# Performance work log

Measured on AMD Instinct MI355X. Metric: run time of the kernel, lower is better.

Reference implementation:

```python
import jax, jax.numpy as jnp
import numpy as np

ROUTINGS = 3
EPS = 1e-9

def squash(s, axis=-1):
    s2 = jnp.sum(s * s, axis=axis, keepdims=True)
    scale = s2 / (1.0 + s2 + EPS)
    return scale * s / jnp.sqrt(s2 + EPS)

def setup_inputs() -> dict:
    key = jax.random.key(0)
    k1, k2 = jax.random.split(key)
    B, N_in, D_in = 64, 2048, 16
    N_out, D_out = 32, 32
    x = jax.random.normal(k1, (B, N_in, D_in), dtype=jnp.float32)
    # glorot-uniform-ish init for W [1, N_in, N_out, D_out, D_in]
    limit = np.sqrt(6.0 / (D_in + D_out)).astype(np.float32)
    W = jax.random.uniform(k2, (1, N_in, N_out, D_out, D_in), dtype=jnp.float32,
                           minval=-limit, maxval=limit)
    return {"x": x, "W": W}

def reference(x, W):
    # u_hat[b,i,j,d] = sum_k W[0,i,j,d,k] * x[b,i,k]   -> [B, N_in, N_out, D_out]
    u_hat = jnp.einsum('bik,ijdk->bijd', x, W[0])
    b = jnp.zeros(u_hat.shape[:-1], dtype=u_hat.dtype)  # [B, N_in, N_out]
    v = None
    for i in range(ROUTINGS):
        c = jax.nn.softmax(b, axis=2)                     # softmax over output capsules
        s = jnp.einsum('bij,bijd->bjd', c, u_hat)         # [B, N_out, D_out]
        v = squash(s)
        if i < ROUTINGS - 1:
            b = b + jnp.einsum('bijd,bjd->bij', u_hat, v)  # agreement update
    return v
```

## Files before the change

### kernel.cpp

```cpp
#include <hip/hip_runtime.h>
#include <cstdint>
#include <cstddef>

#define B_   64
#define NI   2048
#define DI   16
#define NO   32
#define JD   1024
#define IT   16
#define NBX  (NI/IT)
#define XSTR 260
#define EPSQ 1e-9f

typedef __attribute__((ext_vector_type(8)))  short bf16x8;
typedef __attribute__((ext_vector_type(16))) float f32x16;

__device__ __forceinline__ uint32_t pack_split(float w) {
  uint32_t u = __float_as_uint(w);
  float hf = __uint_as_float(u & 0xffff0000u);
  uint32_t lo = __float_as_uint(w - hf) >> 16;
  return (u & 0xffff0000u) | lo;
}

__device__ __forceinline__ void cvt8(const float4 a, const float4 b, bf16x8& h8, bf16x8& l8) {
  float w[8] = {a.x, a.y, a.z, a.w, b.x, b.y, b.z, b.w};
  #pragma unroll
  for (int e = 0; e < 8; ++e) {
    uint32_t u = __float_as_uint(w[e]);
    float hf = __uint_as_float(u & 0xffff0000u);
    h8[e] = (short)(u >> 16);
    l8[e] = (short)(__float_as_uint(w[e] - hf) >> 16);
  }
}

__device__ __forceinline__ f32x16 zero16() {
  f32x16 z;
  #pragma unroll
  for (int r = 0; r < 16; ++r) z[r] = 0.0f;
  return z;
}

template<bool ROUTE>
__global__ __launch_bounds__(512, 2)
void caps_pass(const float* __restrict__ x, const float* __restrict__ W,
               const float* __restrict__ vin, float* __restrict__ part)
{
  __shared__ uint32_t xl[32 * XSTR];
  __shared__ float al[NO * 32];
  __shared__ float cl[NO * 32];

  const int t    = threadIdx.x;
  const int wv   = t >> 6;
  const int l    = t & 63;
  const int col  = l & 31;
  const int hb   = l >> 5;
  const int p    = blockIdx.x;
  const int half = blockIdx.y;
  const int i0   = p * IT;
  const int b0   = half * 32;

  for (int idx = t; idx < 32 * 64; idx += 512) {
    const int bb = idx >> 6, c4 = idx & 63;
    const float4 xv = *reinterpret_cast<const float4*>(
        x + (size_t)(b0 + bb) * (NI * DI) + (size_t)i0 * DI + (c4 << 2));
    uint4 o;
    o.x = pack_split(xv.x); o.y = pack_split(xv.y);
    o.z = pack_split(xv.z); o.w = pack_split(xv.w);
    *reinterpret_cast<uint4*>(&xl[bb * XSTR + (c4 << 2)]) = o;
  }

  float vreg[4][16];
  if constexpr (ROUTE) {
    #pragma unroll
    for (int m = 0; m < 4; ++m)
      #pragma unroll
      for (int r = 0; r < 16; ++r) {
        const int row = (r & 3) + 8 * (r >> 2) + 4 * hb;
        vreg[m][r] = vin[(size_t)(b0 + col) * JD + wv * 128 + m * 32 + row];
      }
  }

  f32x16 sacc[4];
  #pragma unroll
  for (int m = 0; m < 4; ++m) sacc[m] = zero16();

  __syncthreads();

  if constexpr (!ROUTE) {
    for (int ii = 0; ii < IT; ++ii) {
      const uint4 q0 = *reinterpret_cast<const uint4*>(&xl[col * XSTR + (ii << 4) + (hb << 3)]);
      const uint4 q1 = *reinterpret_cast<const uint4*>(&xl[col * XSTR + (ii << 4) + (hb << 3) + 4]);
      bf16x8 xh, xo;
      const uint32_t qq[8] = {q0.x, q0.y, q0.z, q0.w, q1.x, q1.y, q1.z, q1.w};
      #pragma unroll
      for (int e = 0; e < 8; ++e) { xh[e] = (short)(qq[e] >> 16); xo[e] = (short)(qq[e] & 0xffff); }

      const float* wbase = W + (size_t)(i0 + ii) * (JD * DI) + (size_t)wv * 128 * DI;
      #pragma unroll
      for (int m = 0; m < 4; ++m) {
        const float* wt = wbase + m * 32 * DI + col * DI + (hb << 3);
        const float4 wa = *reinterpret_cast<const float4*>(wt);
        const float4 wb = *reinterpret_cast<const float4*>(wt + 4);
        bf16x8 wh, wl; cvt8(wa, wb, wh, wl);
        sacc[m] = __builtin_amdgcn_mfma_f32_32x32x16_bf16(wh, xh, sacc[m], 0, 0, 0);
        sacc[m] = __builtin_amdgcn_mfma_f32_32x32x16_bf16(wh, xo, sacc[m], 0, 0, 0);
        sacc[m] = __builtin_amdgcn_mfma_f32_32x32x16_bf16(wl, xh, sacc[m], 0, 0, 0);
      }
    }
  } else {
    #pragma unroll 1
    for (int ii = 0; ii < IT; ++ii) {
      const uint4 q0 = *reinterpret_cast<const uint4*>(&xl[col * XSTR + (ii << 4) + (hb << 3)]);
      const uint4 q1 = *reinterpret_cast<const uint4*>(&xl[col * XSTR + (ii << 4) + (hb << 3) + 4]);
      bf16x8 xh, xo;
      const uint32_t qq[8] = {q0.x, q0.y, q0.z, q0.w, q1.x, q1.y, q1.z, q1.w};
      #pragma unroll
      for (int e = 0; e < 8; ++e) { xh[e] = (short)(qq[e] >> 16); xo[e] = (short)(qq[e] & 0xffff); }

      const float* wbase = W + (size_t)(i0 + ii) * (JD * DI) + (size_t)wv * 128 * DI;
      f32x16 u[4];
      #pragma unroll
      for (int m = 0; m < 4; ++m) {
        const float* wt = wbase + m * 32 * DI + col * DI + (hb << 3);
        const float4 wa = *reinterpret_cast<const float4*>(wt);
        const float4 wb = *reinterpret_cast<const float4*>(wt + 4);
        bf16x8 wh, wl; cvt8(wa, wb, wh, wl);
        f32x16 c = zero16();
        c = __builtin_amdgcn_mfma_f32_32x32x16_bf16(wh, xh, c, 0, 0, 0);
        c = __builtin_amdgcn_mfma_f32_32x32x16_bf16(wh, xo, c, 0, 0, 0);
        c = __builtin_amdgcn_mfma_f32_32x32x16_bf16(wl, xh, c, 0, 0, 0);
        u[m] = c;
      }

      float ap[4];
      #pragma unroll
      for (int m = 0; m < 4; ++m) {
        float s = 0.f;
        #pragma unroll
        for (int r = 0; r < 16; ++r) s += u[m][r] * vreg[m][r];
        s += __shfl_xor(s, 32);
        ap[m] = s;
      }
      if (l < 32) {
        #pragma unroll
        for (int m = 0; m < 4; ++m) {
          const int j = (wv << 2) + m;
          al[(j << 5) + ((col + j) & 31)] = ap[m];
        }
      }
      __syncthreads();

      {
        const int jj = t & 31;
        #pragma unroll
        for (int rd = 0; rd < 2; ++rd) {
          const int bb = (t >> 5) + (rd << 4);
          const float av = al[(jj << 5) + ((bb + jj) & 31)];
          float mx = av;
          #pragma unroll
          for (int s = 1; s < 32; s <<= 1) mx = fmaxf(mx, __shfl_xor(mx, s, 32));
          const float e = __expf(av - mx);
          float den = e;
          #pragma unroll
          for (int s = 1; s < 32; s <<= 1) den += __shfl_xor(den, s, 32);
          cl[(jj << 5) + ((bb + jj) & 31)] = e / den;
        }
      }
      __syncthreads();

      #pragma unroll
      for (int m = 0; m < 4; ++m) {
        const int j = (wv << 2) + m;
        const float cv = cl[(j << 5) + ((col + j) & 31)];
        #pragma unroll
        for (int r = 0; r < 16; ++r) sacc[m][r] += cv * u[m][r];
      }
    }
  }

  #pragma unroll
  for (int m = 0; m < 4; ++m)
    #pragma unroll
    for (int g = 0; g < 4; ++g) {
      const int jd = (wv << 7) + (m << 5) + (g << 3) + (hb << 2);
      *reinterpret_cast<float4*>(part + (((size_t)(p * B_ + b0 + col)) << 10) + jd) =
          make_float4(sacc[m][4 * g], sacc[m][4 * g + 1], sacc[m][4 * g + 2], sacc[m][4 * g + 3]);
    }
}

__global__ void reduce_squash(const float* __restrict__ part,
                              const float* __restrict__ vprev,
                              float* __restrict__ out, float scale, int addPrev)
{
  const int b   = blockIdx.x;
  const int jd0 = blockIdx.y * 512 + threadIdx.x * 4;

  float4 acc[8];
  #pragma unroll
  for (int u = 0; u < 8; ++u) acc[u] = make_float4(0.f, 0.f, 0.f, 0.f);

  for (int p = 0; p < NBX; p += 8) {
    #pragma unroll
    for (int u = 0; u < 8; ++u) {
      const float4 v = *reinterpret_cast<const float4*>(
          part + (((size_t)((p + u) * B_ + b)) << 10) + jd0);
      acc[u].x += v.x; acc[u].y += v.y; acc[u].z += v.z; acc[u].w += v.w;
    }
  }
  #pragma unroll
  for (int u = 1; u < 8; ++u) {
    acc[0].x += acc[u].x; acc[0].y += acc[u].y;
    acc[0].z += acc[u].z; acc[0].w += acc[u].w;
  }

  float val[4] = {acc[0].x * scale, acc[0].y * scale, acc[0].z * scale, acc[0].w * scale};
  float sq = val[0]*val[0] + val[1]*val[1] + val[2]*val[2] + val[3]*val[3];
  #pragma unroll
  for (int w = 1; w < 8; w <<= 1) sq += __shfl_xor(sq, w, 8);

  const float f = sq / ((1.0f + sq + EPSQ) * sqrtf(sq + EPSQ));
  float4 o = make_float4(f * val[0], f * val[1], f * val[2], f * val[3]);
  if (addPrev) {
    const float4 vp = *reinterpret_cast<const float4*>(vprev + (size_t)b * JD + jd0);
    o.x += vp.x; o.y += vp.y; o.z += vp.z; o.w += vp.w;
  }
  *reinterpret_cast<float4*>(out + (size_t)b * JD + jd0) = o;
}

extern "C" void kernel_launch(void* const* d_in, const int* in_sizes, int n_in,
                              void* d_out, int out_size, void* d_ws, size_t ws_size,
                              hipStream_t stream) {
  const float* x = (const float*)d_in[0];
  const float* W = (const float*)d_in[1];
  float* ws  = (float*)d_ws;
  float* out = (float*)d_out;

  float* partb = ws;
  float* v0    = ws + (size_t)NBX * B_ * JD;
  float* vs    = v0 + B_ * JD;

  const dim3 grid(NBX, 2);
  const dim3 rgrid(B_, 2);
  caps_pass<false><<<grid, 512, 0, stream>>>(x, W, nullptr, partb);
  reduce_squash<<<rgrid, 128, 0, stream>>>(partb, nullptr, v0, 1.0f / 32.0f, 0);
  caps_pass<true><<<grid, 512, 0, stream>>>(x, W, v0, partb);
  reduce_squash<<<rgrid, 128, 0, stream>>>(partb, v0, vs, 1.0f, 1);
  caps_pass<true><<<grid, 512, 0, stream>>>(x, W, vs, partb);
  reduce_squash<<<rgrid, 128, 0, stream>>>(partb, nullptr, out, 1.0f, 0);
}
```

Baseline: 324.5 us.

## Halve input-capsule tile, reorder grid, add atomic-fold fallback for small workspace

Cuts the input capsules per block from 16 to 8, which doubles the grid to 512 blocks and is meant to fill more of the GPU's compute units. The grid is re-indexed so that neighbouring block IDs share a row slab. A fallback path for when the workspace is too small for the doubled partial buffer folds pairs of partials with atomicAdd after a memset. The trade-off is twice as many partial sums for reduce_squash to read, and possibly atomic traffic if the fallback path is taken.

```diff
diff --git a/kernel.cpp b/kernel.cpp
--- a/kernel.cpp
+++ b/kernel.cpp
@@ -7,9 +7,9 @@
 #define DI   16
 #define NO   32
 #define JD   1024
-#define IT   16
+#define IT   8
 #define NBX  (NI/IT)
-#define XSTR 260
+#define XSTR (IT*DI + 4)
 #define EPSQ 1e-9f
 
 typedef __attribute__((ext_vector_type(8)))  short bf16x8;
@@ -40,7 +40,7 @@
   return z;
 }
 
-template<bool ROUTE>
+template<bool ROUTE, bool FOLD>
 __global__ __launch_bounds__(512, 2)
 void caps_pass(const float* __restrict__ x, const float* __restrict__ W,
                const float* __restrict__ vin, float* __restrict__ part)
@@ -54,13 +54,13 @@
   const int l    = t & 63;
   const int col  = l & 31;
   const int hb   = l >> 5;
-  const int p    = blockIdx.x;
-  const int half = blockIdx.y;
+  const int half = blockIdx.x >> 3;
+  const int p    = blockIdx.y * 8 + (blockIdx.x & 7);
   const int i0   = p * IT;
   const int b0   = half * 32;
 
-  for (int idx = t; idx < 32 * 64; idx += 512) {
-    const int bb = idx >> 6, c4 = idx & 63;
+  for (int idx = t; idx < 32 * (IT * DI / 4); idx += 512) {
+    const int bb = idx / (IT * DI / 4), c4 = idx % (IT * DI / 4);
     const float4 xv = *reinterpret_cast<const float4*>(
         x + (size_t)(b0 + bb) * (NI * DI) + (size_t)i0 * DI + (c4 << 2));
     uint4 o;
@@ -178,17 +178,26 @@
     }
   }
 
+  const int pslot = FOLD ? (p >> 1) : p;
   #pragma unroll
   for (int m = 0; m < 4; ++m)
     #pragma unroll
     for (int g = 0; g < 4; ++g) {
       const int jd = (wv << 7) + (m << 5) + (g << 3) + (hb << 2);
-      *reinterpret_cast<float4*>(part + (((size_t)(p * B_ + b0 + col)) << 10) + jd) =
-          make_float4(sacc[m][4 * g], sacc[m][4 * g + 1], sacc[m][4 * g + 2], sacc[m][4 * g + 3]);
-    }
-}
-
-__global__ void reduce_squash(const float* __restrict__ part,
+      float* dst = part + (((size_t)(pslot * B_ + b0 + col)) << 10) + jd;
+      if constexpr (FOLD) {
+        atomicAdd(dst + 0, sacc[m][4 * g]);
+        atomicAdd(dst + 1, sacc[m][4 * g + 1]);
+        atomicAdd(dst + 2, sacc[m][4 * g + 2]);
+        atomicAdd(dst + 3, sacc[m][4 * g + 3]);
+      } else {
+        *reinterpret_cast<float4*>(dst) =
+            make_float4(sacc[m][4 * g], sacc[m][4 * g + 1], sacc[m][4 * g + 2], sacc[m][4 * g + 3]);
+      }
+    }
+}
+
+__global__ void reduce_squash(const float* __restrict__ part, int nPart,
                               const float* __restrict__ vprev,
                               float* __restrict__ out, float scale, int addPrev)
 {
@@ -199,7 +208,7 @@
   #pragma unroll
   for (int u = 0; u < 8; ++u) acc[u] = make_float4(0.f, 0.f, 0.f, 0.f);
 
-  for (int p = 0; p < NBX; p += 8) {
+  for (int p = 0; p < nPart; p += 8) {
     #pragma unroll
     for (int u = 0; u < 8; ++u) {
       const float4 v = *reinterpret_cast<const float4*>(
@@ -235,16 +244,34 @@
   float* ws  = (float*)d_ws;
   float* out = (float*)d_out;
 
-  float* partb = ws;
-  float* v0    = ws + (size_t)NBX * B_ * JD;
-  float* vs    = v0 + B_ * JD;
-
-  const dim3 grid(NBX, 2);
+  const dim3 grid(16, NBX / 8);
   const dim3 rgrid(B_, 2);
-  caps_pass<false><<<grid, 512, 0, stream>>>(x, W, nullptr, partb);
-  reduce_squash<<<rgrid, 128, 0, stream>>>(partb, nullptr, v0, 1.0f / 32.0f, 0);
-  caps_pass<true><<<grid, 512, 0, stream>>>(x, W, v0, partb);
-  reduce_squash<<<rgrid, 128, 0, stream>>>(partb, v0, vs, 1.0f, 1);
-  caps_pass<true><<<grid, 512, 0, stream>>>(x, W, vs, partb);
-  reduce_squash<<<rgrid, 128, 0, stream>>>(partb, nullptr, out, 1.0f, 0);
-}
+  const size_t needFull = ((size_t)NBX * B_ * JD + 2u * B_ * JD) * sizeof(float);
+
+  if (ws_size >= needFull) {
+    float* partb = ws;
+    float* v0    = ws + (size_t)NBX * B_ * JD;
+    float* vs    = v0 + B_ * JD;
+    caps_pass<false, false><<<grid, 512, 0, stream>>>(x, W, nullptr, partb);
+    reduce_squash<<<rgrid, 128, 0, stream>>>(partb, NBX, nullptr, v0, 1.0f / 32.0f, 0);
+    caps_pass<true, false><<<grid, 512, 0, stream>>>(x, W, v0, partb);
+    reduce_squash<<<rgrid, 128, 0, stream>>>(partb, NBX, v0, vs, 1.0f, 1);
+    caps_pass<true, false><<<grid, 512, 0, stream>>>(x, W, vs, partb);
+    reduce_squash<<<rgrid, 128, 0, stream>>>(partb, NBX, nullptr, out, 1.0f, 0);
+  } else {
+    const int nslots = NBX / 2;
+    float* partb = ws;
+    float* v0    = ws + (size_t)nslots * B_ * JD;
+    float* vs    = v0 + B_ * JD;
+    const size_t pbytes = (size_t)nslots * B_ * JD * sizeof(float);
+    hipMemsetAsync(partb, 0, pbytes, stream);
+    caps_pass<false, true><<<grid, 512, 0, stream>>>(x, W, nullptr, partb);
+    reduce_squash<<<rgrid, 128, 0, stream>>>(partb, nslots, nullptr, v0, 1.0f / 32.0f, 0);
+    hipMemsetAsync(partb, 0, pbytes, stream);
+    caps_pass<true, true><<<grid, 512, 0, stream>>>(x, W, v0, partb);
+    reduce_squash<<<rgrid, 128, 0, stream>>>(partb, nslots, v0, vs, 1.0f, 1);
+    hipMemsetAsync(partb, 0, pbytes, stream);
+    caps_pass<true, true><<<grid, 512, 0, stream>>>(x, W, vs, partb);
+    reduce_squash<<<rgrid, 128, 0, stream>>>(partb, nslots, nullptr, out, 1.0f, 0);
+  }
+}
```

After: 388.2 us. +19.6%, slower.
